# Performance work log

Measured on AMD Instinct MI355X. Metric: run time of the kernel, lower is better.

Reference implementation:

```python
import jax, jax.numpy as jnp
import numpy as np

B, L, IN_DIM, D, H, NCONV = 64, 400, 500, 128, 8, 4
HD = D // H  # head dim = 16


def _conv1d(x, w, b, pad, groups=1):
    # x: [B, L, Cin], w: [k, Cin//groups, Cout]
    y = jax.lax.conv_general_dilated(
        x, w, window_strides=(1,), padding=[(pad, pad)],
        dimension_numbers=('NWC', 'WIO', 'NWC'), feature_group_count=groups)
    return y + b


def _layernorm(x, g, b, eps=1e-5):
    mu = jnp.mean(x, axis=-1, keepdims=True)
    var = jnp.mean(jnp.square(x - mu), axis=-1, keepdims=True)
    return (x - mu) * jax.lax.rsqrt(var + eps) * g + b


def _posenc(L, d):
    pos = jnp.arange(L, dtype=jnp.float32)[:, None]                 # [L,1]
    div = jnp.exp(jnp.arange(0, d, 2, dtype=jnp.float32) * (-jnp.log(10000.0) / d))
    ang = pos * div                                                 # [L, d/2]
    return jnp.stack([jnp.sin(ang), jnp.cos(ang)], axis=-1).reshape(L, d)


def setup_inputs() -> dict:
    key = jax.random.key(0)
    ks = jax.random.split(key, 24)
    s = lambda k, shape, scale: jax.random.normal(k, shape, dtype=jnp.float32) * scale
    inp = {
        'x': s(ks[0], (B, L, IN_DIM), 1.0),
        # init conv: k=5, 500 -> 128
        'w_init': s(ks[1], (5, IN_DIM, D), 0.02),
        'b_init': jnp.zeros((D,), jnp.float32),
        # 4 depthwise-separable conv layers (pre-LN, residual): depthwise k=7
        'ln_conv_g': jnp.ones((NCONV, D), jnp.float32),
        'ln_conv_b': jnp.zeros((NCONV, D), jnp.float32),
        'w_dw': s(ks[2], (NCONV, 7, 1, D), 0.1),
        'b_dw': jnp.zeros((NCONV, D), jnp.float32),
        'w_pw': s(ks[3], (NCONV, 1, D, D), 0.05),
        'b_pw': jnp.zeros((NCONV, D), jnp.float32),
        # self-attention (pre-LN, residual)
        'ln_att_g': jnp.ones((D,), jnp.float32),
        'ln_att_b': jnp.zeros((D,), jnp.float32),
        'wq': s(ks[4], (D, D), 0.05), 'bq': jnp.zeros((D,), jnp.float32),
        'wk': s(ks[5], (D, D), 0.05), 'bk': jnp.zeros((D,), jnp.float32),
        'wv': s(ks[6], (D, D), 0.05), 'bv': jnp.zeros((D,), jnp.float32),
        'wo': s(ks[7], (D, D), 0.05), 'bo': jnp.zeros((D,), jnp.float32),
        # FFN (pre-LN, residual)
        'ln_ffn_g': jnp.ones((D,), jnp.float32),
        'ln_ffn_b': jnp.zeros((D,), jnp.float32),
        'w1': s(ks[8], (D, D), 0.05), 'b1': jnp.zeros((D,), jnp.float32),
        'w2': s(ks[9], (D, D), 0.05), 'b2': jnp.zeros((D,), jnp.float32),
    }
    return inp


def reference(x, w_init, b_init, ln_conv_g, ln_conv_b, w_dw, b_dw, w_pw, b_pw,
              ln_att_g, ln_att_b, wq, bq, wk, bk, wv, bv, wo, bo,
              ln_ffn_g, ln_ffn_b, w1, b1, w2, b2):
    # 1) init conv (Conv1d k=5 pad=2, 500 -> 128); torch permutes, equivalent NWC conv
    h = _conv1d(x, w_init, b_init, pad=2)                    # [B, L, D]
    # 2) positional encoding
    h = h + _posenc(h.shape[1], D)
    for i in range(NCONV):
        res = h
        h = _layernorm(h, ln_conv_g[i], ln_conv_b[i])
        h = _conv1d(h, w_dw[i], b_dw[i], pad=3, groups=D)    # depthwise k=7
        h = _conv1d(h, w_pw[i], b_pw[i], pad=0)              # pointwise 1x1
        h = jax.nn.relu(h) + res
    # 4) multi-head self-attention, pre-LN + residual
    res = h
    hn = _layernorm(h, ln_att_g, ln_att_b)
    q = (hn @ wq + bq).reshape(B, L, H, HD)
    k = (hn @ wk + bk).reshape(B, L, H, HD)
    v = (hn @ wv + bv).reshape(B, L, H, HD)
    scores = jnp.einsum('bqhd,bkhd->bhqk', q, k) / jnp.sqrt(jnp.float32(HD))
    attn = jax.nn.softmax(scores, axis=-1)
    o = jnp.einsum('bhqk,bkhd->bqhd', attn, v).reshape(B, L, D)
    h = o @ wo + bo + res
    # 5) FFN, pre-LN + residual
    res = h
    hn = _layernorm(h, ln_ffn_g, ln_ffn_b)
    h = jax.nn.relu(hn @ w1 + b1) @ w2 + b2 + res
    return h
```

## Files before the change

### kernel.cpp

```cpp
#include <hip/hip_runtime.h>
#include <hip/hip_bf16.h>
#include <math.h>

#define B 64
#define L 400
#define IN_DIM 500
#define D 128
#define H 8
#define HD 16
#define NCONV 4
#define BL (B*L)

typedef __attribute__((ext_vector_type(8))) unsigned short ushort8;
typedef __attribute__((ext_vector_type(8))) short bf16x8;
typedef __attribute__((ext_vector_type(4))) float f32x4;

__device__ __forceinline__ unsigned short f2bf(float f) {
    unsigned u = __float_as_uint(f);
    unsigned r = (u + 0x7fffu + ((u >> 16) & 1u)) >> 16;
    return (unsigned short)r;
}
__device__ __forceinline__ float bf2f(unsigned short u) {
    return __uint_as_float(((unsigned)u) << 16);
}

__device__ __forceinline__ void gload16(const void* g, void* l) {
    __builtin_amdgcn_global_load_lds(
        (const __attribute__((address_space(1))) unsigned int*)g,
        (__attribute__((address_space(3))) unsigned int*)l,
        16, 0, 0);
}

__global__ __launch_bounds__(256) void k_cvt_x(
        const float* __restrict__ x, unsigned short* __restrict__ xb) {
    int idx = blockIdx.x * 256 + threadIdx.x;
    int row = idx >> 6, ch = idx & 63;
    int b = row / 404, rr = row - b * 404;
    ushort8 o = (ushort8)0;
    if (rr >= 2 && rr < 402) {
        int l = rr - 2;
        const float* src = x + ((size_t)b * 400 + l) * 500 + ch * 8;
        if (ch < 62) {
            float4 v0 = *(const float4*)(src);
            float4 v1 = *(const float4*)(src + 4);
            o[0] = f2bf(v0.x); o[1] = f2bf(v0.y); o[2] = f2bf(v0.z); o[3] = f2bf(v0.w);
            o[4] = f2bf(v1.x); o[5] = f2bf(v1.y); o[6] = f2bf(v1.z); o[7] = f2bf(v1.w);
        } else {
#pragma unroll
            for (int j = 0; j < 8; ++j) {
                int c = ch * 8 + j;
                o[j] = (c < 500) ? f2bf(src[j]) : (unsigned short)0;
            }
        }
    }
    *(ushort8*)(xb + (size_t)idx * 8) = o;
}

__global__ __launch_bounds__(256) void k_cvt_w(
        const float* __restrict__ w, unsigned short* __restrict__ wbt) {
    int idx = blockIdx.x * 256 + threadIdx.x;
    int k = idx & 511, n = (idx >> 9) & 127, t = idx >> 16;
    float v = (k < 500) ? w[((size_t)t * 500 + k) * 128 + n] : 0.f;
    wbt[idx] = f2bf(v);
}

__global__ __launch_bounds__(256) void k_cvt_wall(
        const float* w0, const float* w1, const float* w2, const float* w3,
        const float* w4, const float* w5, const float* w6, const float* w7,
        const float* w8, const float* w9, unsigned short* __restrict__ out) {
    const float* arr[10] = {w0,w1,w2,w3,w4,w5,w6,w7,w8,w9};
    int widx = blockIdx.x >> 6;
    const float* w = arr[widx];
    int idx = ((blockIdx.x & 63) << 8) + threadIdx.x;
    int n = idx >> 7, k = idx & 127;
    out[(size_t)widx * 16384 + idx] = f2bf(w[k * 128 + n]);
}

#define TM 80
#define BK 64
__global__ __launch_bounds__(256) void k_initconv_mfma(
        const unsigned short* __restrict__ xb,
        const unsigned short* __restrict__ wbt,
        const float* __restrict__ bias, float* __restrict__ out) {
    __shared__ unsigned short As[84 * BK];
    __shared__ unsigned short Ws[5][64 * BK];
    int tid = threadIdx.x;
    int b = blockIdx.x / 10;
    int rem = blockIdx.x - b * 10;
    int l0 = (rem >> 1) * TM;
    int nh = rem & 1;
    int lane = tid & 63, wave = tid >> 6;
    int kgrp = lane >> 4, lm = lane & 15;

    f32x4 acc[5];
#pragma unroll
    for (int mf = 0; mf < 5; ++mf) acc[mf] = (f32x4)0.f;

    const unsigned short* abase = xb + ((size_t)(b * 404 + l0)) * 512;
    const unsigned short* wbase = wbt + (size_t)nh * 64 * 512;

    for (int k0 = 0; k0 < 512; k0 += BK) {
        for (int idx = tid; idx < 672; idx += 256) {
            int r = idx >> 3, sc = idx & 7;
            gload16(abase + (size_t)r * 512 + k0 + ((sc ^ (r & 7)) * 8),
                    As + idx * 8);
        }
#pragma unroll
        for (int i = 0; i < 10; ++i) {
            int idx = tid + i * 256;
            int t = idx >> 9;
            int sub = idx & 511;
            int n = sub >> 3, sc = sub & 7;
            gload16(wbase + (size_t)t * 128 * 512 + (size_t)n * 512 + k0
                        + ((sc ^ (n & 7)) * 8),
                    &Ws[t][0] + sub * 8);
        }
        __syncthreads();
        int n16 = wave * 16 + lm;
#pragma unroll
        for (int ks = 0; ks < 2; ++ks) {
            int gc = ks * 4 + kgrp;
            bf16x8 bfr[5];
#pragma unroll
            for (int t = 0; t < 5; ++t)
                bfr[t] = *(const bf16x8*)(&Ws[t][0] + n16 * 64
                                          + ((gc ^ (n16 & 7)) * 8));
#pragma unroll
            for (int mf = 0; mf < 5; ++mf) {
#pragma unroll
                for (int t = 0; t < 5; ++t) {
                    int r = mf * 16 + lm + t;
                    bf16x8 af = *(const bf16x8*)(As + r * 64
                                                 + ((gc ^ (r & 7)) * 8));
                    acc[mf] = __builtin_amdgcn_mfma_f32_16x16x32_bf16(
                        af, bfr[t], acc[mf], 0, 0, 0);
                }
            }
        }
        __syncthreads();
    }

    {
        int n = nh * 64 + wave * 16 + lm;
        float bs = bias[n];
        float pbase = expf(-(float)(n & ~1) * (9.210340371976184f / 128.0f));
#pragma unroll
        for (int mf = 0; mf < 5; ++mf) {
#pragma unroll
            for (int r = 0; r < 4; ++r) {
                int l = l0 + mf * 16 + kgrp * 4 + r;
                float ang = (float)l * pbase;
                float pe = (n & 1) ? cosf(ang) : sinf(ang);
                out[((size_t)b * 400 + l) * 128 + n] = acc[mf][r] + bs + pe;
            }
        }
    }
}

__global__ __launch_bounds__(256) void k_ln(
        const float* __restrict__ in, const float* __restrict__ g,
        const float* __restrict__ bta, unsigned short* __restrict__ out) {
    int wave = threadIdx.x >> 6, lane = threadIdx.x & 63;
    size_t row = (size_t)blockIdx.x * 4 + wave;
    const float* p = in + row * D;
    float2 v = *(const float2*)(p + lane * 2);
    float s = v.x + v.y;
    float q = v.x * v.x + v.y * v.y;
#pragma unroll
    for (int off = 32; off; off >>= 1) {
        s += __shfl_xor(s, off);
        q += __shfl_xor(q, off);
    }
    float mu  = s * (1.f / 128.f);
    float var = q * (1.f / 128.f) - mu * mu;
    float inv = rsqrtf(var + 1e-5f);
    float2 gg = *(const float2*)(g + lane * 2);
    float2 bb = *(const float2*)(bta + lane * 2);
    float ox = (v.x - mu) * inv * gg.x + bb.x;
    float oy = (v.y - mu) * inv * gg.y + bb.y;
    unsigned pk = (unsigned)f2bf(ox) | ((unsigned)f2bf(oy) << 16);
    *(unsigned*)(out + row * D + lane * 2) = pk;
}

__global__ __launch_bounds__(256) void k_dw(
        const unsigned short* __restrict__ in, const float* __restrict__ w,
        const float* __restrict__ bias, unsigned short* __restrict__ out) {
    __shared__ float s[22 * D];
    int tid = threadIdx.x;
    int b  = blockIdx.x / 25;
    int l0 = (blockIdx.x - b * 25) * 16;
    for (int idx = tid; idx < 22 * 16; idx += 256) {
        int r = idx >> 4, c = idx & 15;
        int gl = l0 - 3 + r;
        float vals[8];
        if (gl >= 0 && gl < L) {
            ushort8 u = *(const ushort8*)(in + ((size_t)b * L + gl) * D + c * 8);
#pragma unroll
            for (int j = 0; j < 8; ++j) vals[j] = bf2f(u[j]);
        } else {
#pragma unroll
            for (int j = 0; j < 8; ++j) vals[j] = 0.f;
        }
#pragma unroll
        for (int j = 0; j < 8; ++j) s[r * D + c * 8 + j] = vals[j];
    }
    __syncthreads();
    int d = tid & 127, half = tid >> 7;
    float wr[7];
#pragma unroll
    for (int t = 0; t < 7; ++t) wr[t] = w[t * D + d];
    float bs = bias[d];
    for (int jj = 0; jj < 8; ++jj) {
        int lj = half * 8 + jj;
        float a = bs;
#pragma unroll
        for (int t = 0; t < 7; ++t) a = fmaf(s[(lj + t) * D + d], wr[t], a);
        out[((size_t)b * L + l0 + lj) * D + d] = f2bf(a);
    }
}

__global__ __launch_bounds__(256) void k_gemm_bf16(
        const unsigned short* __restrict__ A,
        const unsigned short* __restrict__ Wt,
        const float* __restrict__ bias,
        const float* __restrict__ res,
        float* __restrict__ outf,
        unsigned short* __restrict__ outb,
        int relu, float oscale) {
    __shared__ unsigned short As[32 * 128];
    __shared__ unsigned short Ws[128 * 128];
    int tid = threadIdx.x;
    int m0 = blockIdx.x * 32;
    int lane = tid & 63, wave = tid >> 6;
    int lm = lane & 15, kgrp = lane >> 4;
    int wm = wave >> 1, wn = wave & 1;

#pragma unroll
    for (int i = 0; i < 2; ++i) {
        int idx = tid + i * 256;
        int r = idx >> 4, sc = idx & 15;
        gload16(A + ((size_t)(m0 + r)) * 128 + ((sc ^ (r & 15)) * 8), As + idx * 8);
    }
#pragma unroll
    for (int i = 0; i < 8; ++i) {
        int idx = tid + i * 256;
        int n = idx >> 4, sc = idx & 15;
        gload16(Wt + ((size_t)n) * 128 + ((sc ^ (n & 15)) * 8), Ws + idx * 8);
    }
    __syncthreads();

    f32x4 acc[4];
#pragma unroll
    for (int nt = 0; nt < 4; ++nt) acc[nt] = (f32x4)0.f;

#pragma unroll
    for (int kc = 0; kc < 4; ++kc) {
        int c = kc * 4 + kgrp;
        int r = wm * 16 + lm;
        bf16x8 af = *(const bf16x8*)(As + (r * 16 + (c ^ (r & 15))) * 8);
#pragma unroll
        for (int nt = 0; nt < 4; ++nt) {
            int n = wn * 64 + nt * 16 + lm;
            bf16x8 bfv = *(const bf16x8*)(Ws + (n * 16 + (c ^ (n & 15))) * 8);
            acc[nt] = __builtin_amdgcn_mfma_f32_16x16x32_bf16(af, bfv, acc[nt], 0, 0, 0);
        }
    }

#pragma unroll
    for (int nt = 0; nt < 4; ++nt) {
        int n = wn * 64 + nt * 16 + lm;
        float bs = bias[n];
#pragma unroll
        for (int r = 0; r < 4; ++r) {
            size_t m = (size_t)m0 + wm * 16 + kgrp * 4 + r;
            float v = acc[nt][r] + bs;
            if (relu) v = fmaxf(v, 0.f);
            if (res)  v += res[m * 128 + n];
            if (outf) outf[m * 128 + n] = v;
            else      outb[m * 128 + n] = f2bf(v * oscale);
        }
    }
}

#define KS 40
#define VS 424
__global__ __launch_bounds__(256) void k_attn_mfma(
        const unsigned short* __restrict__ qb,
        const unsigned short* __restrict__ kb,
        const unsigned short* __restrict__ vb,
        unsigned short* __restrict__ out) {
    __shared__ __align__(16) unsigned short Kpad[400 * KS];
    __shared__ __align__(16) unsigned short Vt[16 * VS];
    __shared__ __align__(16) unsigned short Ptmp[4][16 * KS];
    int tid = threadIdx.x;
    int b = blockIdx.x >> 3, h = blockIdx.x & 7;
    int lane = tid & 63, wave = tid >> 6;
    int lm = lane & 15, kgrp = lane >> 4;

    for (int idx = tid; idx < 800; idx += 256) {
        int l = idx >> 1, half = idx & 1;
        ushort8 kv = *(const ushort8*)(kb + ((size_t)(b * 400 + l)) * 128 + h * 16 + half * 8);
        *(ushort8*)(Kpad + l * KS + half * 8) = kv;
        *(ushort8*)(Kpad + l * KS + 16 + half * 8) = (ushort8)0;
    }
    for (int idx = tid; idx < 800; idx += 256) {
        int kk = idx >> 1, dh = idx & 1;
        ushort8 vv = *(const ushort8*)(vb + ((size_t)(b * 400 + kk)) * 128 + h * 16 + dh * 8);
#pragma unroll
        for (int j = 0; j < 8; ++j) Vt[(dh * 8 + j) * VS + kk] = vv[j];
    }
    {
        int d = tid >> 4, kk = 400 + (tid & 15);
        Vt[d * VS + kk] = 0;
    }
    __syncthreads();

    unsigned short* Pw = Ptmp[wave];
    for (int tt = wave; tt < 25; tt += 4) {
        int q0 = tt * 16;
        bf16x8 Qf = *(const bf16x8*)(qb + ((size_t)(b * 400 + q0 + lm)) * 128 + h * 16 + kgrp * 8);
        f32x4 s[25];
#pragma unroll
        for (int kt = 0; kt < 25; ++kt) {
            bf16x8 Kf = *(const bf16x8*)(Kpad + (kt * 16 + lm) * KS + kgrp * 8);
            s[kt] = __builtin_amdgcn_mfma_f32_16x16x32_bf16(Qf, Kf, (f32x4)0.f, 0, 0, 0);
        }
        float rmax[4], rsum[4];
#pragma unroll
        for (int r = 0; r < 4; ++r) rmax[r] = -1e30f;
#pragma unroll
        for (int kt = 0; kt < 25; ++kt)
#pragma unroll
            for (int r = 0; r < 4; ++r) rmax[r] = fmaxf(rmax[r], s[kt][r]);
#pragma unroll
        for (int mask = 1; mask <= 8; mask <<= 1)
#pragma unroll
            for (int r = 0; r < 4; ++r) rmax[r] = fmaxf(rmax[r], __shfl_xor(rmax[r], mask));
#pragma unroll
        for (int r = 0; r < 4; ++r) rsum[r] = 0.f;
#pragma unroll
        for (int kt = 0; kt < 25; ++kt)
#pragma unroll
            for (int r = 0; r < 4; ++r) {
                float p = __expf(s[kt][r] - rmax[r]);
                s[kt][r] = p;
                rsum[r] += p;
            }
#pragma unroll
        for (int mask = 1; mask <= 8; mask <<= 1)
#pragma unroll
            for (int r = 0; r < 4; ++r) rsum[r] += __shfl_xor(rsum[r], mask);
        float rinv[4];
#pragma unroll
        for (int r = 0; r < 4; ++r) rinv[r] = 1.f / rsum[r];

        f32x4 O = (f32x4)0.f;
#pragma unroll
        for (int kc = 0; kc < 13; ++kc) {
#pragma unroll
            for (int t = 0; t < 2; ++t) {
                int kt = kc * 2 + t;
#pragma unroll
                for (int r = 0; r < 4; ++r) {
                    unsigned short pv = (kt < 25) ? f2bf(s[kt][r]) : (unsigned short)0;
                    Pw[(kgrp * 4 + r) * KS + t * 16 + lm] = pv;
                }
            }
            __builtin_amdgcn_wave_barrier();
            __builtin_amdgcn_s_waitcnt(0);
            __builtin_amdgcn_wave_barrier();
            bf16x8 Pf = *(const bf16x8*)(Pw + lm * KS + kgrp * 8);
            bf16x8 Vf = *(const bf16x8*)(Vt + lm * VS + kc * 32 + kgrp * 8);
            O = __builtin_amdgcn_mfma_f32_16x16x32_bf16(Pf, Vf, O, 0, 0, 0);
            __builtin_amdgcn_wave_barrier();
        }
#pragma unroll
        for (int r = 0; r < 4; ++r) {
            int q = q0 + kgrp * 4 + r;
            out[((size_t)(b * 400 + q)) * 128 + h * 16 + lm] = f2bf(O[r] * rinv[r]);
        }
    }
}

extern "C" void kernel_launch(void* const* d_in, const int* in_sizes, int n_in,
                              void* d_out, int out_size, void* d_ws, size_t ws_size,
                              hipStream_t stream) {
    (void)in_sizes; (void)n_in; (void)out_size; (void)ws_size;
    const float* x      = (const float*)d_in[0];
    const float* w_init = (const float*)d_in[1];
    const float* b_init = (const float*)d_in[2];
    const float* lncg   = (const float*)d_in[3];
    const float* lncb   = (const float*)d_in[4];
    const float* w_dw   = (const float*)d_in[5];
    const float* b_dw   = (const float*)d_in[6];
    const float* w_pw   = (const float*)d_in[7];
    const float* b_pw   = (const float*)d_in[8];
    const float* lnag   = (const float*)d_in[9];
    const float* lnab   = (const float*)d_in[10];
    const float* wq     = (const float*)d_in[11];
    const float* bq     = (const float*)d_in[12];
    const float* wk     = (const float*)d_in[13];
    const float* bk     = (const float*)d_in[14];
    const float* wv     = (const float*)d_in[15];
    const float* bv     = (const float*)d_in[16];
    const float* wo     = (const float*)d_in[17];
    const float* bo     = (const float*)d_in[18];
    const float* lnfg   = (const float*)d_in[19];
    const float* lnfb   = (const float*)d_in[20];
    const float* w1     = (const float*)d_in[21];
    const float* b1     = (const float*)d_in[22];
    const float* w2     = (const float*)d_in[23];
    const float* b2     = (const float*)d_in[24];

    float* ws = (float*)d_ws;
    const size_t NBL = (size_t)BL * D;
    float* h0 = ws;
    float* outp = (float*)d_out;

    unsigned short* hnb = (unsigned short*)(ws + NBL);
    unsigned short* t0b = hnb + NBL;
    unsigned short* qb  = t0b + NBL;
    unsigned short* kb  = qb + NBL;
    unsigned short* vb  = kb + NBL;
    unsigned short* wt  = vb + NBL;
    unsigned short* xb  = wt + 10 * 16384;
    unsigned short* wbt = xb + (size_t)64 * 404 * 512;

    k_cvt_x<<<6464, 256, 0, stream>>>(x, xb);
    k_cvt_w<<<1280, 256, 0, stream>>>(w_init, wbt);
    k_cvt_wall<<<640, 256, 0, stream>>>(
        w_pw, w_pw + 16384, w_pw + 2 * 16384, w_pw + 3 * 16384,
        wq, wk, wv, wo, w1, w2, wt);

    k_initconv_mfma<<<640, 256, 0, stream>>>(xb, wbt, b_init, h0);

    for (int i = 0; i < NCONV; ++i) {
        k_ln<<<6400, 256, 0, stream>>>(h0, lncg + i * D, lncb + i * D, hnb);
        k_dw<<<1600, 256, 0, stream>>>(hnb, w_dw + (size_t)i * 7 * D, b_dw + i * D, t0b);
        k_gemm_bf16<<<800, 256, 0, stream>>>(t0b, wt + (size_t)i * 16384,
                                             b_pw + i * D, h0, h0, nullptr, 1, 1.f);
    }

    k_ln<<<6400, 256, 0, stream>>>(h0, lnag, lnab, hnb);
    k_gemm_bf16<<<800, 256, 0, stream>>>(hnb, wt + 4 * 16384, bq, nullptr,
                                         nullptr, qb, 0, 0.25f);
    k_gemm_bf16<<<800, 256, 0, stream>>>(hnb, wt + 5 * 16384, bk, nullptr,
                                         nullptr, kb, 0, 1.f);
    k_gemm_bf16<<<800, 256, 0, stream>>>(hnb, wt + 6 * 16384, bv, nullptr,
                                         nullptr, vb, 0, 1.f);
    k_attn_mfma<<<512, 256, 0, stream>>>(qb, kb, vb, t0b);
    k_gemm_bf16<<<800, 256, 0, stream>>>(t0b, wt + 7 * 16384, bo, h0,
                                         h0, nullptr, 0, 1.f);

    k_ln<<<6400, 256, 0, stream>>>(h0, lnfg, lnfb, hnb);
    k_gemm_bf16<<<800, 256, 0, stream>>>(hnb, wt + 8 * 16384, b1, nullptr,
                                         nullptr, t0b, 1, 1.f);
    k_gemm_bf16<<<800, 256, 0, stream>>>(t0b, wt + 9 * 16384, b2, h0,
                                         outp, nullptr, 0, 1.f);
}
```

Baseline: 362.3 us.

## Fuse LN, depthwise conv and pointwise GEMM per conv block; fuse LN into QKV/FFN GEMMs

Each conv layer becomes a single kernel. It layernorms a 38-row halo tile into LDS, runs the depthwise k=7 conv into a swizzled LDS tile, then does the pointwise 1x1 MFMA GEMM with relu and residual. Output ping-pongs between two fp32 buffers. Separately, the attention and FFN layernorms are fused into the following GEMM, and the Q/K/V projections share one launch that reuses the normalized A tile across three weight matrices. This removes many launches and the bf16 intermediate round-trips to global memory, at the cost of recomputing LN on halo rows and more LDS per block, which may lower occupancy.

```diff
diff --git a/kernel.cpp b/kernel.cpp
--- a/kernel.cpp
+++ b/kernel.cpp
@@ -157,65 +157,217 @@
     }
 }
 
-__global__ __launch_bounds__(256) void k_ln(
-        const float* __restrict__ in, const float* __restrict__ g,
-        const float* __restrict__ bta, unsigned short* __restrict__ out) {
-    int wave = threadIdx.x >> 6, lane = threadIdx.x & 63;
-    size_t row = (size_t)blockIdx.x * 4 + wave;
-    const float* p = in + row * D;
-    float2 v = *(const float2*)(p + lane * 2);
-    float s = v.x + v.y;
-    float q = v.x * v.x + v.y * v.y;
-#pragma unroll
-    for (int off = 32; off; off >>= 1) {
-        s += __shfl_xor(s, off);
-        q += __shfl_xor(q, off);
-    }
-    float mu  = s * (1.f / 128.f);
-    float var = q * (1.f / 128.f) - mu * mu;
-    float inv = rsqrtf(var + 1e-5f);
-    float2 gg = *(const float2*)(g + lane * 2);
-    float2 bb = *(const float2*)(bta + lane * 2);
-    float ox = (v.x - mu) * inv * gg.x + bb.x;
-    float oy = (v.y - mu) * inv * gg.y + bb.y;
-    unsigned pk = (unsigned)f2bf(ox) | ((unsigned)f2bf(oy) << 16);
-    *(unsigned*)(out + row * D + lane * 2) = pk;
-}
-
-__global__ __launch_bounds__(256) void k_dw(
-        const unsigned short* __restrict__ in, const float* __restrict__ w,
-        const float* __restrict__ bias, unsigned short* __restrict__ out) {
-    __shared__ float s[22 * D];
+#define CB_ROWS 38
+__global__ __launch_bounds__(256) void k_convblock(
+        const float* __restrict__ hin, float* __restrict__ hout,
+        const float* __restrict__ lng, const float* __restrict__ lnb,
+        const float* __restrict__ wdw, const float* __restrict__ bdw,
+        const unsigned short* __restrict__ wpt, const float* __restrict__ bpw) {
+    __shared__ unsigned short Ws[128 * 128];
+    __shared__ unsigned short Ln[CB_ROWS * 128];
+    __shared__ unsigned short Dw[32 * 128];
     int tid = threadIdx.x;
-    int b  = blockIdx.x / 25;
-    int l0 = (blockIdx.x - b * 25) * 16;
-    for (int idx = tid; idx < 22 * 16; idx += 256) {
-        int r = idx >> 4, c = idx & 15;
-        int gl = l0 - 3 + r;
-        float vals[8];
-        if (gl >= 0 && gl < L) {
-            ushort8 u = *(const ushort8*)(in + ((size_t)b * L + gl) * D + c * 8);
-#pragma unroll
-            for (int j = 0; j < 8; ++j) vals[j] = bf2f(u[j]);
-        } else {
-#pragma unroll
-            for (int j = 0; j < 8; ++j) vals[j] = 0.f;
-        }
-#pragma unroll
-        for (int j = 0; j < 8; ++j) s[r * D + c * 8 + j] = vals[j];
+    int b = blockIdx.x / 13;
+    int tile = blockIdx.x - b * 13;
+    int l0 = tile * 32;
+    int lv = (l0 + 32 <= L) ? 32 : (L - l0);
+    int lane = tid & 63, wave = tid >> 6;
+    int lm = lane & 15, kgrp = lane >> 4;
+
+#pragma unroll
+    for (int i = 0; i < 8; ++i) {
+        int idx = tid + i * 256;
+        int n = idx >> 4, sc = idx & 15;
+        gload16(wpt + (size_t)n * 128 + ((sc ^ (n & 15)) * 8), Ws + idx * 8);
+    }
+
+    {
+        float2 gg = *(const float2*)(lng + lane * 2);
+        float2 bb = *(const float2*)(lnb + lane * 2);
+#pragma unroll
+        for (int ri = 0; ri < 10; ++ri) {
+            int r = wave + ri * 4;
+            if (r < CB_ROWS) {
+                int gl = l0 - 3 + r;
+                bool ok = (gl >= 0 && gl < L);
+                float2 v = make_float2(0.f, 0.f);
+                if (ok) v = *(const float2*)(hin + ((size_t)b * L + gl) * 128 + lane * 2);
+                float s = v.x + v.y, q = v.x * v.x + v.y * v.y;
+#pragma unroll
+                for (int off = 32; off; off >>= 1) {
+                    s += __shfl_xor(s, off);
+                    q += __shfl_xor(q, off);
+                }
+                float mu  = s * (1.f / 128.f);
+                float var = q * (1.f / 128.f) - mu * mu;
+                float inv = rsqrtf(var + 1e-5f);
+                unsigned pk = 0;
+                if (ok) {
+                    float ox = (v.x - mu) * inv * gg.x + bb.x;
+                    float oy = (v.y - mu) * inv * gg.y + bb.y;
+                    pk = (unsigned)f2bf(ox) | ((unsigned)f2bf(oy) << 16);
+                }
+                *(unsigned*)(Ln + r * 128 + lane * 2) = pk;
+            }
+        }
     }
     __syncthreads();
-    int d = tid & 127, half = tid >> 7;
-    float wr[7];
-#pragma unroll
-    for (int t = 0; t < 7; ++t) wr[t] = w[t * D + d];
-    float bs = bias[d];
-    for (int jj = 0; jj < 8; ++jj) {
-        int lj = half * 8 + jj;
-        float a = bs;
-#pragma unroll
-        for (int t = 0; t < 7; ++t) a = fmaf(s[(lj + t) * D + d], wr[t], a);
-        out[((size_t)b * L + l0 + lj) * D + d] = f2bf(a);
+
+    {
+        int d = tid & 127, half = tid >> 7;
+        float wr[7];
+#pragma unroll
+        for (int t = 0; t < 7; ++t) wr[t] = wdw[t * 128 + d];
+        float bs = bdw[d];
+        float win[7];
+#pragma unroll
+        for (int t = 0; t < 6; ++t) win[t] = bf2f(Ln[(half * 16 + t) * 128 + d]);
+#pragma unroll
+        for (int lj = 0; lj < 16; ++lj) {
+            int l = half * 16 + lj;
+            win[6] = bf2f(Ln[(l + 6) * 128 + d]);
+            float a = bs;
+#pragma unroll
+            for (int t = 0; t < 7; ++t) a = fmaf(win[t], wr[t], a);
+#pragma unroll
+            for (int t = 0; t < 6; ++t) win[t] = win[t + 1];
+            Dw[l * 128 + ((d >> 3) ^ (l & 15)) * 8 + (d & 7)] = f2bf(a);
+        }
+    }
+    __syncthreads();
+
+    f32x4 acc[2][2];
+#pragma unroll
+    for (int mf = 0; mf < 2; ++mf)
+#pragma unroll
+        for (int nt = 0; nt < 2; ++nt) acc[mf][nt] = (f32x4)0.f;
+#pragma unroll
+    for (int kc = 0; kc < 4; ++kc) {
+        int c = kc * 4 + kgrp;
+        bf16x8 af[2];
+#pragma unroll
+        for (int mf = 0; mf < 2; ++mf) {
+            int r = mf * 16 + lm;
+            af[mf] = *(const bf16x8*)(Dw + r * 128 + (c ^ (r & 15)) * 8);
+        }
+#pragma unroll
+        for (int nt = 0; nt < 2; ++nt) {
+            int n = wave * 32 + nt * 16 + lm;
+            bf16x8 bfv = *(const bf16x8*)(Ws + n * 128 + (c ^ (n & 15)) * 8);
+#pragma unroll
+            for (int mf = 0; mf < 2; ++mf)
+                acc[mf][nt] = __builtin_amdgcn_mfma_f32_16x16x32_bf16(
+                    af[mf], bfv, acc[mf][nt], 0, 0, 0);
+        }
+    }
+
+#pragma unroll
+    for (int nt = 0; nt < 2; ++nt) {
+        int n = wave * 32 + nt * 16 + lm;
+        float bsn = bpw[n];
+#pragma unroll
+        for (int mf = 0; mf < 2; ++mf) {
+#pragma unroll
+            for (int r = 0; r < 4; ++r) {
+                int row = mf * 16 + kgrp * 4 + r;
+                if (row < lv) {
+                    size_t gi = ((size_t)b * L + l0 + row) * 128 + n;
+                    hout[gi] = fmaxf(acc[mf][nt][r] + bsn, 0.f) + hin[gi];
+                }
+            }
+        }
+    }
+}
+
+__global__ __launch_bounds__(256) void k_ln_gemm(
+        const float* __restrict__ h, const float* __restrict__ g,
+        const float* __restrict__ bta, const unsigned short* __restrict__ wt0,
+        int nw, const float* __restrict__ bias0, const float* __restrict__ bias1,
+        const float* __restrict__ bias2, unsigned short* __restrict__ out0,
+        unsigned short* __restrict__ out1, unsigned short* __restrict__ out2,
+        float s0, int relu) {
+    __shared__ unsigned short As[32 * 128];
+    __shared__ unsigned short Ws[128 * 128];
+    int tid = threadIdx.x;
+    int m0 = blockIdx.x * 32;
+    int lane = tid & 63, wave = tid >> 6;
+    int lm = lane & 15, kgrp = lane >> 4;
+    int wm = wave >> 1, wn = wave & 1;
+
+#pragma unroll
+    for (int i = 0; i < 8; ++i) {
+        int idx = tid + i * 256;
+        int n = idx >> 4, sc = idx & 15;
+        gload16(wt0 + (size_t)n * 128 + ((sc ^ (n & 15)) * 8), Ws + idx * 8);
+    }
+
+    {
+        float2 gg = *(const float2*)(g + lane * 2);
+        float2 bb = *(const float2*)(bta + lane * 2);
+#pragma unroll
+        for (int ri = 0; ri < 8; ++ri) {
+            int r = wave + ri * 4;
+            float2 v = *(const float2*)(h + ((size_t)m0 + r) * 128 + lane * 2);
+            float s = v.x + v.y, q = v.x * v.x + v.y * v.y;
+#pragma unroll
+            for (int off = 32; off; off >>= 1) {
+                s += __shfl_xor(s, off);
+                q += __shfl_xor(q, off);
+            }
+            float mu  = s * (1.f / 128.f);
+            float var = q * (1.f / 128.f) - mu * mu;
+            float inv = rsqrtf(var + 1e-5f);
+            float ox = (v.x - mu) * inv * gg.x + bb.x;
+            float oy = (v.y - mu) * inv * gg.y + bb.y;
+            unsigned pk = (unsigned)f2bf(ox) | ((unsigned)f2bf(oy) << 16);
+            *(unsigned*)(As + r * 128 + ((lane >> 2) ^ (r & 15)) * 8
+                         + ((lane * 2) & 7)) = pk;
+        }
+    }
+
+    for (int i = 0; i < nw; ++i) {
+        __syncthreads();
+        f32x4 acc[4];
+#pragma unroll
+        for (int nt = 0; nt < 4; ++nt) acc[nt] = (f32x4)0.f;
+#pragma unroll
+        for (int kc = 0; kc < 4; ++kc) {
+            int c = kc * 4 + kgrp;
+            int r = wm * 16 + lm;
+            bf16x8 af = *(const bf16x8*)(As + r * 128 + (c ^ (r & 15)) * 8);
+#pragma unroll
+            for (int nt = 0; nt < 4; ++nt) {
+                int n = wn * 64 + nt * 16 + lm;
+                bf16x8 bfv = *(const bf16x8*)(Ws + n * 128 + (c ^ (n & 15)) * 8);
+                acc[nt] = __builtin_amdgcn_mfma_f32_16x16x32_bf16(
+                    af, bfv, acc[nt], 0, 0, 0);
+            }
+        }
+        const float* bias = (i == 0) ? bias0 : (i == 1) ? bias1 : bias2;
+        unsigned short* out = (i == 0) ? out0 : (i == 1) ? out1 : out2;
+        float sc0 = (i == 0) ? s0 : 1.f;
+#pragma unroll
+        for (int nt = 0; nt < 4; ++nt) {
+            int n = wn * 64 + nt * 16 + lm;
+            float bsn = bias[n];
+#pragma unroll
+            for (int r = 0; r < 4; ++r) {
+                size_t m = (size_t)m0 + wm * 16 + kgrp * 4 + r;
+                float v = acc[nt][r] + bsn;
+                if (relu) v = fmaxf(v, 0.f);
+                out[m * 128 + n] = f2bf(v * sc0);
+            }
+        }
+        if (i + 1 < nw) {
+            __syncthreads();
+            const unsigned short* wp = wt0 + (size_t)(i + 1) * 16384;
+#pragma unroll
+            for (int j = 0; j < 8; ++j) {
+                int idx = tid + j * 256;
+                int n = idx >> 4, sc = idx & 15;
+                gload16(wp + (size_t)n * 128 + ((sc ^ (n & 15)) * 8), Ws + idx * 8);
+            }
+        }
     }
 }
 
@@ -425,6 +577,7 @@
     unsigned short* wt  = vb + NBL;
     unsigned short* xb  = wt + 10 * 16384;
     unsigned short* wbt = xb + (size_t)64 * 404 * 512;
+    float* h1 = (float*)(wbt + (size_t)5 * 128 * 512);
 
     k_cvt_x<<<6464, 256, 0, stream>>>(x, xb);
     k_cvt_w<<<1280, 256, 0, stream>>>(w_init, wbt);
@@ -435,26 +588,23 @@
     k_initconv_mfma<<<640, 256, 0, stream>>>(xb, wbt, b_init, h0);
 
     for (int i = 0; i < NCONV; ++i) {
-        k_ln<<<6400, 256, 0, stream>>>(h0, lncg + i * D, lncb + i * D, hnb);
-        k_dw<<<1600, 256, 0, stream>>>(hnb, w_dw + (size_t)i * 7 * D, b_dw + i * D, t0b);
-        k_gemm_bf16<<<800, 256, 0, stream>>>(t0b, wt + (size_t)i * 16384,
-                                             b_pw + i * D, h0, h0, nullptr, 1, 1.f);
-    }
-
-    k_ln<<<6400, 256, 0, stream>>>(h0, lnag, lnab, hnb);
-    k_gemm_bf16<<<800, 256, 0, stream>>>(hnb, wt + 4 * 16384, bq, nullptr,
-                                         nullptr, qb, 0, 0.25f);
-    k_gemm_bf16<<<800, 256, 0, stream>>>(hnb, wt + 5 * 16384, bk, nullptr,
-                                         nullptr, kb, 0, 1.f);
-    k_gemm_bf16<<<800, 256, 0, stream>>>(hnb, wt + 6 * 16384, bv, nullptr,
-                                         nullptr, vb, 0, 1.f);
+        const float* hin = (i & 1) ? h1 : h0;
+        float* hout      = (i & 1) ? h0 : h1;
+        k_convblock<<<832, 256, 0, stream>>>(
+            hin, hout, lncg + i * D, lncb + i * D,
+            w_dw + (size_t)i * 7 * D, b_dw + i * D,
+            wt + (size_t)i * 16384, b_pw + i * D);
+    }
+
+    k_ln_gemm<<<800, 256, 0, stream>>>(h0, lnag, lnab, wt + 4 * 16384, 3,
+                                       bq, bk, bv, qb, kb, vb, 0.25f, 0);
     k_attn_mfma<<<512, 256, 0, stream>>>(qb, kb, vb, t0b);
     k_gemm_bf16<<<800, 256, 0, stream>>>(t0b, wt + 7 * 16384, bo, h0,
                                          h0, nullptr, 0, 1.f);
 
-    k_ln<<<6400, 256, 0, stream>>>(h0, lnfg, lnfb, hnb);
-    k_gemm_bf16<<<800, 256, 0, stream>>>(hnb, wt + 8 * 16384, b1, nullptr,
-                                         nullptr, t0b, 1, 1.f);
+    k_ln_gemm<<<800, 256, 0, stream>>>(h0, lnfg, lnfb, wt + 8 * 16384, 1,
+                                       b1, nullptr, nullptr,
+                                       t0b, nullptr, nullptr, 1.f, 1);
     k_gemm_bf16<<<800, 256, 0, stream>>>(t0b, wt + 9 * 16384, b2, h0,
                                          outp, nullptr, 0, 1.f);
 }
```

New measurement: 341.0 us. 5.9% less time.
